# Performance work log

Measured on AMD Instinct MI355X. Metric: run time of the kernel, lower is better.

The kernel has to match this reference:

```python
import jax, jax.numpy as jnp
import numpy as np

HEADS = 4
DIM_HEAD = 32


def setup_inputs() -> dict:
    key = jax.random.key(0)
    k1, k2, k3, k4 = jax.random.split(key, 4)
    b, dim, t = 8, 64, 16384
    inner = HEADS * DIM_HEAD  # 128
    x = jax.random.normal(k1, (b, dim, t), dtype=jnp.float32)
    # Conv1d(dim, inner*3, kernel=1, bias=False) -> weight (3*inner, dim)
    w_qkv = jax.random.normal(k2, (3 * inner, dim), dtype=jnp.float32) * (1.0 / np.sqrt(dim))
    # Conv1d(inner, dim, kernel=1) -> weight (dim, inner), bias (dim,)
    w_out = jax.random.normal(k3, (dim, inner), dtype=jnp.float32) * (1.0 / np.sqrt(inner))
    b_out = jax.random.normal(k4, (dim,), dtype=jnp.float32) * 0.01
    return {"x": x, "w_qkv": w_qkv, "w_out": w_out, "b_out": b_out}


def reference(x, w_qkv, w_out, b_out):
    b, c, t = x.shape
    h, dh = HEADS, DIM_HEAD
    # 1x1 conv == per-timestep matmul: (b, 3*inner, t)
    qkv = jnp.einsum('oc,bct->bot', w_qkv, x)
    q, k, v = jnp.split(qkv, 3, axis=1)
    q = q.reshape(b, h, dh, t)
    k = k.reshape(b, h, dh, t)
    v = v.reshape(b, h, dh, t)
    q = jax.nn.softmax(q, axis=-1)   # softmax over time
    k = jax.nn.softmax(k, axis=-2)   # softmax over head-dim d
    # einsum('bhdt,bhds->bhds', k, v): sums k over t, broadcast-scales v
    context = jnp.einsum('bhdt,bhds->bhds', k, v)
    # einsum('bhdt,bhds->bhdt', q, context): sums context over s, scales q
    out = jnp.einsum('bhdt,bhds->bhdt', q, context)
    out = out.reshape(b, h * dh, t)
    # to_out 1x1 conv with bias
    return jnp.einsum('oc,bct->bot', w_out, out) + b_out[None, :, None]
```

## Files before the change

### kernel.cpp

```cpp
#include <hip/hip_runtime.h>
#include <math.h>


typedef short short8 __attribute__((ext_vector_type(8)));
typedef short short4s __attribute__((ext_vector_type(4)));
typedef float f32x4 __attribute__((ext_vector_type(4)));

namespace {
constexpr int NB = 8;
constexpr int NC = 64;
constexpr int NT = 16384;
constexpr int NI = 128;
constexpr int TBK = 256;
constexpr int CPB = NT / TBK;
constexpr int NBLK = NB * CPB;
constexpr int XSP = 72;
constexpr int PTP = 136;
constexpr int PT  = 32;

constexpr int F_ZQ = 0;
constexpr int F_KS = NI;
constexpr int F_XS = 2 * NI;
constexpr int SLOT = 2 * NI + NC;
constexpr int WS_NFLOAT = NB * CPB * SLOT;
}

__device__ __forceinline__ unsigned short f2bf(float f) {
  unsigned u = __float_as_uint(f);
  u += 0x7fffu + ((u >> 16) & 1u);
  return (unsigned short)(u >> 16);
}

template <bool XS>
__device__ __forceinline__ void stage_x(const float* __restrict__ xb, int t0,
                                        unsigned short* xs, float* xsum_dst, int tid) {
  const int c = tid >> 2, tq = tid & 3;
  const float4* xr = (const float4*)(xb + (size_t)c * NT + t0);
  float s = 0.f;
#pragma unroll 4
  for (int i = 0; i < TBK / 16; ++i) {
    const int tv = tq + 4 * i;
    float4 v = xr[tv];
    if (XS) s += (v.x + v.y) + (v.z + v.w);
    const int t = 4 * tv;
    xs[(t + 0) * XSP + c] = f2bf(v.x);
    xs[(t + 1) * XSP + c] = f2bf(v.y);
    xs[(t + 2) * XSP + c] = f2bf(v.z);
    xs[(t + 3) * XSP + c] = f2bf(v.w);
  }
  if (XS) {
    s += __shfl_xor(s, 1, 64);
    s += __shfl_xor(s, 2, 64);
    if (tq == 0) xsum_dst[c] = s;
  }
}

__device__ __forceinline__ void load_aq(const float* __restrict__ wqkv, int w,
                                        int lm, int quad, short8 aq[2][2]) {
#pragma unroll
  for (int tile = 0; tile < 2; ++tile)
#pragma unroll
    for (int s = 0; s < 2; ++s) {
      const float* pq = wqkv + (size_t)(32 * w + tile * 16 + lm) * NC + s * 32 + quad * 8;
#pragma unroll
      for (int j = 0; j < 8; ++j) aq[tile][s][j] = (short)f2bf(pq[j]);
    }
}

__global__ __launch_bounds__(256) void la_stats(
    const float* __restrict__ x, const float* __restrict__ wqkv,
    float* __restrict__ ws)
{
  __shared__ __align__(16) unsigned short xs[TBK * XSP];

  const int bid = blockIdx.x;
  const int b = bid >> 6, chunk = bid & 63;
  const int tid = threadIdx.x, lane = tid & 63;
  const int w = __builtin_amdgcn_readfirstlane(tid >> 6);
  const int lm = lane & 15, quad = lane >> 4;
  const float* xb = x + (size_t)b * NC * NT;
  float* slot = ws + (size_t)(b * CPB + chunk) * SLOT;

  stage_x<true>(xb, chunk * TBK, xs, slot + F_XS, tid);

  short8 aq[2][2], ak[2][2];
  load_aq(wqkv, w, lm, quad, aq);
#pragma unroll
  for (int tile = 0; tile < 2; ++tile)
#pragma unroll
    for (int s = 0; s < 2; ++s) {
      const float* pk = wqkv + (size_t)(NI + 32 * w + tile * 16 + lm) * NC + s * 32 + quad * 8;
#pragma unroll
      for (int j = 0; j < 8; ++j) ak[tile][s][j] = (short)f2bf(pk[j]);
    }

  float zq_acc[2][4] = {};
  float ks_acc[2][4] = {};
  __syncthreads();

  for (int tc = 0; tc < TBK / 16; ++tc) {
    short8 bf[2];
#pragma unroll
    for (int s = 0; s < 2; ++s)
      bf[s] = *(const short8*)&xs[(tc * 16 + lm) * XSP + s * 32 + quad * 8];
    f32x4 cq[2] = {{0,0,0,0},{0,0,0,0}}, ck[2] = {{0,0,0,0},{0,0,0,0}};
#pragma unroll
    for (int tile = 0; tile < 2; ++tile)
#pragma unroll
      for (int s = 0; s < 2; ++s) {
        cq[tile] = __builtin_amdgcn_mfma_f32_16x16x32_bf16(aq[tile][s], bf[s], cq[tile], 0, 0, 0);
        ck[tile] = __builtin_amdgcn_mfma_f32_16x16x32_bf16(ak[tile][s], bf[s], ck[tile], 0, 0, 0);
      }
    float ke[2][4];
    float zt = 0.f;
#pragma unroll
    for (int tile = 0; tile < 2; ++tile)
#pragma unroll
      for (int r = 0; r < 4; ++r) {
        zq_acc[tile][r] += __expf(cq[tile][r]);
        float e = __expf(ck[tile][r]);
        ke[tile][r] = e;
        zt += e;
      }
    zt += __shfl_xor(zt, 16, 64);
    zt += __shfl_xor(zt, 32, 64);
    const float rz = __builtin_amdgcn_rcpf(zt);
#pragma unroll
    for (int tile = 0; tile < 2; ++tile)
#pragma unroll
      for (int r = 0; r < 4; ++r)
        ks_acc[tile][r] = fmaf(ke[tile][r], rz, ks_acc[tile][r]);
  }

#pragma unroll
  for (int tile = 0; tile < 2; ++tile)
#pragma unroll
    for (int r = 0; r < 4; ++r) {
      float a = zq_acc[tile][r], k = ks_acc[tile][r];
#pragma unroll
      for (int off = 1; off < 16; off <<= 1) {
        a += __shfl_xor(a, off, 64);
        k += __shfl_xor(k, off, 64);
      }
      if (lm == 0) {
        const int c = 32 * w + tile * 16 + quad * 4 + r;
        slot[F_ZQ + c] = a;
        slot[F_KS + c] = k;
      }
    }
}

__global__ __launch_bounds__(256) void la_out(
    const float* __restrict__ x, const float* __restrict__ wqkv,
    const float* __restrict__ wout, const float* __restrict__ bout,
    const float* __restrict__ ws, float* __restrict__ y)
{
  __shared__ __align__(16) unsigned short xs[TBK * XSP];
  __shared__ __align__(16) unsigned short pt[PT * PTP];
  __shared__ float scale_s[NI];
  __shared__ float xsum_s[NC];

  const int bid = blockIdx.x;
  const int b = bid >> 6, chunk = bid & 63;
  const int tid = threadIdx.x, lane = tid & 63;
  const int w = __builtin_amdgcn_readfirstlane(tid >> 6);
  const int lm = lane & 15, quad = lane >> 4;
  const int t0 = chunk * TBK;
  const float* xb = x + (size_t)b * NC * NT;
  const float* wsb = ws + (size_t)b * CPB * SLOT;

  stage_x<false>(xb, t0, xs, nullptr, tid);

  if (tid < NC) {
    float s = 0.f;
#pragma unroll 8
    for (int sl = 0; sl < CPB; ++sl) s += wsb[(size_t)sl * SLOT + F_XS + tid];
    xsum_s[tid] = s;
  }
  __syncthreads();
  if (tid < NI) {
    float vs = 0.f;
    const float* wv = wqkv + (size_t)(2 * NI + tid) * NC;
#pragma unroll 8
    for (int cc = 0; cc < NC; ++cc) vs = fmaf(wv[cc], xsum_s[cc], vs);
    float zq_t = 0.f, ks_t = 0.f;
#pragma unroll 8
    for (int sl = 0; sl < CPB; ++sl) {
      zq_t += wsb[(size_t)sl * SLOT + F_ZQ + tid];
      ks_t += wsb[(size_t)sl * SLOT + F_KS + tid];
    }
    scale_s[tid] = ks_t * vs / zq_t;
  }
  __syncthreads();

  short8 aq[2][2];
  load_aq(wqkv, w, lm, quad, aq);
  short8 aw[4];
  {
    const int o = 16 * w + lm;
#pragma unroll
    for (int s = 0; s < 4; ++s) {
      const float* wo = wout + (size_t)o * NI + s * 32 + quad * 8;
#pragma unroll
      for (int j = 0; j < 8; ++j)
        aw[s][j] = (short)f2bf(wo[j] * scale_s[s * 32 + quad * 8 + j]);
    }
  }
  float bias[4];
#pragma unroll
  for (int r = 0; r < 4; ++r) bias[r] = bout[16 * w + quad * 4 + r];

  for (int sub = 0; sub < TBK / PT; ++sub) {
    for (int tc = 0; tc < PT / 16; ++tc) {
      const int tl = sub * PT + tc * 16;
      short8 bf[2];
#pragma unroll
      for (int s = 0; s < 2; ++s)
        bf[s] = *(const short8*)&xs[(tl + lm) * XSP + s * 32 + quad * 8];
      f32x4 cq[2] = {{0,0,0,0},{0,0,0,0}};
#pragma unroll
      for (int tile = 0; tile < 2; ++tile)
#pragma unroll
        for (int s = 0; s < 2; ++s)
          cq[tile] = __builtin_amdgcn_mfma_f32_16x16x32_bf16(aq[tile][s], bf[s], cq[tile], 0, 0, 0);
#pragma unroll
      for (int tile = 0; tile < 2; ++tile) {
        short4s pv;
#pragma unroll
        for (int r = 0; r < 4; ++r) pv[r] = (short)f2bf(__expf(cq[tile][r]));
        *(short4s*)&pt[(tc * 16 + lm) * PTP + 32 * w + tile * 16 + quad * 4] = pv;
      }
    }
    __syncthreads();
    for (int tc = 0; tc < PT / 16; ++tc) {
      short8 bp[4];
#pragma unroll
      for (int s = 0; s < 4; ++s)
        bp[s] = *(const short8*)&pt[(tc * 16 + lm) * PTP + s * 32 + quad * 8];
      f32x4 acc = {bias[0], bias[1], bias[2], bias[3]};
#pragma unroll
      for (int s = 0; s < 4; ++s)
        acc = __builtin_amdgcn_mfma_f32_16x16x32_bf16(aw[s], bp[s], acc, 0, 0, 0);
#pragma unroll
      for (int r = 0; r < 4; ++r)
        y[((size_t)b * NC + 16 * w + quad * 4 + r) * NT + t0 + sub * PT + tc * 16 + lm] = acc[r];
    }
    __syncthreads();
  }
}

extern "C" void kernel_launch(void* const* d_in, const int* in_sizes, int n_in,
                              void* d_out, int out_size, void* d_ws, size_t ws_size,
                              hipStream_t stream)
{
  const float* x    = (const float*)d_in[0];
  const float* wqkv = (const float*)d_in[1];
  const float* wout = (const float*)d_in[2];
  const float* bout = (const float*)d_in[3];
  float* y  = (float*)d_out;
  float* ws = (float*)d_ws;

  if (ws_size < (size_t)WS_NFLOAT * sizeof(float)) return;

  la_stats<<<dim3(NBLK), 256, 0, stream>>>(x, wqkv, ws);
  la_out<<<dim3(NBLK), 256, 0, stream>>>(x, wqkv, wout, bout, ws, y);
}
```

Baseline: 116.6 us.

## Materialize exp(q) tile in workspace instead of recomputing in output kernel

The stats kernel now writes bf16 exp(q) values for every timestep and channel to a large workspace buffer. The output kernel no longer restages x or recomputes the q projection and exponentials; it just loads the precomputed P tile into shared memory and runs the output GEMM. This trades redundant MFMA and exp work, plus a second read of x, for an extra 32MB write and read of intermediate data.

```diff
diff --git a/kernel.cpp b/kernel.cpp
--- a/kernel.cpp
+++ b/kernel.cpp
@@ -23,6 +23,8 @@
 constexpr int F_XS = 2 * NI;
 constexpr int SLOT = 2 * NI + NC;
 constexpr int WS_NFLOAT = NB * CPB * SLOT;
+constexpr size_t P_ELEMS = (size_t)NB * NT * NI;
+constexpr size_t WS_BYTES_NEEDED = (size_t)WS_NFLOAT * 4 + P_ELEMS * 2;
 }
 
 __device__ __forceinline__ unsigned short f2bf(float f) {
@@ -31,7 +33,6 @@
   return (unsigned short)(u >> 16);
 }
 
-template <bool XS>
 __device__ __forceinline__ void stage_x(const float* __restrict__ xb, int t0,
                                         unsigned short* xs, float* xsum_dst, int tid) {
   const int c = tid >> 2, tq = tid & 3;
@@ -41,18 +42,16 @@
   for (int i = 0; i < TBK / 16; ++i) {
     const int tv = tq + 4 * i;
     float4 v = xr[tv];
-    if (XS) s += (v.x + v.y) + (v.z + v.w);
+    s += (v.x + v.y) + (v.z + v.w);
     const int t = 4 * tv;
     xs[(t + 0) * XSP + c] = f2bf(v.x);
     xs[(t + 1) * XSP + c] = f2bf(v.y);
     xs[(t + 2) * XSP + c] = f2bf(v.z);
     xs[(t + 3) * XSP + c] = f2bf(v.w);
   }
-  if (XS) {
-    s += __shfl_xor(s, 1, 64);
-    s += __shfl_xor(s, 2, 64);
-    if (tq == 0) xsum_dst[c] = s;
-  }
+  s += __shfl_xor(s, 1, 64);
+  s += __shfl_xor(s, 2, 64);
+  if (tq == 0) xsum_dst[c] = s;
 }
 
 __device__ __forceinline__ void load_aq(const float* __restrict__ wqkv, int w,
@@ -80,8 +79,10 @@
   const int lm = lane & 15, quad = lane >> 4;
   const float* xb = x + (size_t)b * NC * NT;
   float* slot = ws + (size_t)(b * CPB + chunk) * SLOT;
-
-  stage_x<true>(xb, chunk * TBK, xs, slot + F_XS, tid);
+  unsigned short* Pb = (unsigned short*)(ws + WS_NFLOAT)
+                       + (size_t)(b * CPB + chunk) * TBK * NI;
+
+  stage_x(xb, chunk * TBK, xs, slot + F_XS, tid);
 
   short8 aq[2][2], ak[2][2];
   load_aq(wqkv, w, lm, quad, aq);
@@ -114,14 +115,19 @@
     float ke[2][4];
     float zt = 0.f;
 #pragma unroll
-    for (int tile = 0; tile < 2; ++tile)
+    for (int tile = 0; tile < 2; ++tile) {
+      short4s pv;
 #pragma unroll
       for (int r = 0; r < 4; ++r) {
-        zq_acc[tile][r] += __expf(cq[tile][r]);
+        float eq = __expf(cq[tile][r]);
+        zq_acc[tile][r] += eq;
+        pv[r] = (short)f2bf(eq);
         float e = __expf(ck[tile][r]);
         ke[tile][r] = e;
         zt += e;
       }
+      *(short4s*)&Pb[(size_t)(tc * 16 + lm) * NI + 32 * w + tile * 16 + quad * 4] = pv;
+    }
     zt += __shfl_xor(zt, 16, 64);
     zt += __shfl_xor(zt, 32, 64);
     const float rz = __builtin_amdgcn_rcpf(zt);
@@ -150,13 +156,12 @@
     }
 }
 
-__global__ __launch_bounds__(256) void la_out(
-    const float* __restrict__ x, const float* __restrict__ wqkv,
-    const float* __restrict__ wout, const float* __restrict__ bout,
-    const float* __restrict__ ws, float* __restrict__ y)
+__global__ __launch_bounds__(256) void la_gemm(
+    const float* __restrict__ wqkv, const float* __restrict__ wout,
+    const float* __restrict__ bout, const float* __restrict__ ws,
+    float* __restrict__ y)
 {
-  __shared__ __align__(16) unsigned short xs[TBK * XSP];
-  __shared__ __align__(16) unsigned short pt[PT * PTP];
+  __shared__ __align__(16) unsigned short ptile[PT * PTP];
   __shared__ float scale_s[NI];
   __shared__ float xsum_s[NC];
 
@@ -166,10 +171,9 @@
   const int w = __builtin_amdgcn_readfirstlane(tid >> 6);
   const int lm = lane & 15, quad = lane >> 4;
   const int t0 = chunk * TBK;
-  const float* xb = x + (size_t)b * NC * NT;
   const float* wsb = ws + (size_t)b * CPB * SLOT;
-
-  stage_x<false>(xb, t0, xs, nullptr, tid);
+  const unsigned short* Pb = (const unsigned short*)(ws + WS_NFLOAT)
+                             + (size_t)(b * CPB + chunk) * TBK * NI;
 
   if (tid < NC) {
     float s = 0.f;
@@ -193,8 +197,6 @@
   }
   __syncthreads();
 
-  short8 aq[2][2];
-  load_aq(wqkv, w, lm, quad, aq);
   short8 aw[4];
   {
     const int o = 16 * w + lm;
@@ -210,33 +212,21 @@
 #pragma unroll
   for (int r = 0; r < 4; ++r) bias[r] = bout[16 * w + quad * 4 + r];
 
+  const int tl0 = tid >> 4;
+  const int coff = (tid & 15) * 8;
   for (int sub = 0; sub < TBK / PT; ++sub) {
-    for (int tc = 0; tc < PT / 16; ++tc) {
-      const int tl = sub * PT + tc * 16;
-      short8 bf[2];
-#pragma unroll
-      for (int s = 0; s < 2; ++s)
-        bf[s] = *(const short8*)&xs[(tl + lm) * XSP + s * 32 + quad * 8];
-      f32x4 cq[2] = {{0,0,0,0},{0,0,0,0}};
-#pragma unroll
-      for (int tile = 0; tile < 2; ++tile)
-#pragma unroll
-        for (int s = 0; s < 2; ++s)
-          cq[tile] = __builtin_amdgcn_mfma_f32_16x16x32_bf16(aq[tile][s], bf[s], cq[tile], 0, 0, 0);
-#pragma unroll
-      for (int tile = 0; tile < 2; ++tile) {
-        short4s pv;
-#pragma unroll
-        for (int r = 0; r < 4; ++r) pv[r] = (short)f2bf(__expf(cq[tile][r]));
-        *(short4s*)&pt[(tc * 16 + lm) * PTP + 32 * w + tile * 16 + quad * 4] = pv;
-      }
+#pragma unroll
+    for (int i = 0; i < 2; ++i) {
+      const int tl = i * 16 + tl0;
+      short8 v = *(const short8*)&Pb[(size_t)(sub * PT + tl) * NI + coff];
+      *(short8*)&ptile[tl * PTP + coff] = v;
     }
     __syncthreads();
     for (int tc = 0; tc < PT / 16; ++tc) {
       short8 bp[4];
 #pragma unroll
       for (int s = 0; s < 4; ++s)
-        bp[s] = *(const short8*)&pt[(tc * 16 + lm) * PTP + s * 32 + quad * 8];
+        bp[s] = *(const short8*)&ptile[(tc * 16 + lm) * PTP + s * 32 + quad * 8];
       f32x4 acc = {bias[0], bias[1], bias[2], bias[3]};
 #pragma unroll
       for (int s = 0; s < 4; ++s)
@@ -260,8 +250,8 @@
   float* y  = (float*)d_out;
   float* ws = (float*)d_ws;
 
-  if (ws_size < (size_t)WS_NFLOAT * sizeof(float)) return;
+  if (ws_size < WS_BYTES_NEEDED) return;
 
   la_stats<<<dim3(NBLK), 256, 0, stream>>>(x, wqkv, ws);
-  la_out<<<dim3(NBLK), 256, 0, stream>>>(x, wqkv, wout, bout, ws, y);
-}
+  la_gemm<<<dim3(NBLK), 256, 0, stream>>>(wqkv, wout, bout, ws, y);
+}
```

Result: no change. 117.6 us (+0.8%).
